# Performance work log

Hardware: AMD Instinct MI355X
Metric: run time of the kernel (lower is better)

## Reference

```python
import jax, jax.numpy as jnp
import numpy as np

IN_DIM = 256
OUT_DIM = 256
B, N, E = 8, 1024, 262144
K_RATIO = 0.5
BN_EPS = 1e-5


def _xavier(key, shape):
    fan_in, fan_out = shape[1], shape[0]
    lim = float(np.sqrt(6.0 / (fan_in + fan_out)))
    return jax.random.uniform(key, shape, jnp.float32, -lim, lim)


def setup_inputs() -> dict:
    key = jax.random.key(0)
    ks = jax.random.split(key, 10)
    x = jax.random.normal(ks[0], (B, N, IN_DIM), jnp.float32)
    edges = jax.random.randint(ks[1], (2, E), 0, B * N, jnp.int64 if jax.config.jax_enable_x64 else jnp.int32)
    return {
        "x": x,
        "edges": edges,
        "att_proj_w": _xavier(ks[2], (OUT_DIM, IN_DIM)),
        "att_proj_b": jnp.zeros((OUT_DIM,), jnp.float32),
        "att_map_w": _xavier(ks[3], (1, OUT_DIM)).reshape(OUT_DIM),
        "pwa_w": _xavier(ks[4], (OUT_DIM, IN_DIM)),
        "pwa_b": jnp.zeros((OUT_DIM,), jnp.float32),
        "pwo_w": _xavier(ks[5], (OUT_DIM, IN_DIM)),
        "pwo_b": jnp.zeros((OUT_DIM,), jnp.float32),
        "bn_gamma": jnp.ones((OUT_DIM,), jnp.float32),
        "bn_beta": jnp.zeros((OUT_DIM,), jnp.float32),
        "y_w": _xavier(ks[6], (1, OUT_DIM)).reshape(OUT_DIM),
        "y_b": jnp.zeros((), jnp.float32),
    }


def reference(x, edges, att_proj_w, att_proj_b, att_map_w, pwa_w, pwa_b,
              pwo_w, pwo_b, bn_gamma, bn_beta, y_w, y_b):
    b, n, d = x.shape
    num_nodes = b * n
    xf = x.reshape(num_nodes, d)
    src, dst = edges[0], edges[1]  # x_j = source, x_i = destination

    # --- GAT message: alpha = att_map(tanh(att_proj(x_i * x_j))) ---
    x_j = xf[src]                                # [E, d]
    x_i = xf[dst]                                # [E, d]
    h = jnp.tanh((x_i * x_j) @ att_proj_w.T + att_proj_b)  # [E, out]
    alpha = h @ att_map_w                        # [E]

    # --- segment softmax over destination nodes ---
    amax = jax.ops.segment_max(alpha, dst, num_segments=num_nodes)
    a = jnp.exp(alpha - amax[dst])
    denom = jax.ops.segment_sum(a, dst, num_segments=num_nodes)
    w = a / (denom[dst] + 1e-16)

    # --- scatter-sum aggregate of alpha * x_j ---
    agg = jax.ops.segment_sum(w[:, None] * x_j, dst, num_segments=num_nodes)  # [num_nodes, d]

    out = agg @ pwa_w.T + pwa_b + xf @ pwo_w.T + pwo_b  # [num_nodes, out]

    # --- BatchNorm1d (training-mode batch stats, biased var) + SELU ---
    mean = out.mean(axis=0)
    var = out.var(axis=0)
    out = (out - mean) * jax.lax.rsqrt(var + BN_EPS) * bn_gamma + bn_beta
    out = jax.nn.selu(out)

    out = out.reshape(b, n, -1)  # [B, N, out]

    # --- GraphPool: top-k by sigmoid score, gate by score ---
    y = jax.nn.sigmoid(out @ y_w + y_b)  # [B, N]
    k = max(int(n * K_RATIO), 1)
    vals, ids = jax.lax.top_k(y, k)      # [B, k]
    x_top = jnp.take_along_axis(out, ids[..., None], axis=1)  # [B, k, out]
    return x_top * vals[..., None]
```

## Files before the change

### kernel.cpp

```cpp
#include <hip/hip_runtime.h>
#include <math.h>

#define NODES 8192
#define NEDGE 262144
#define DIM 256

typedef float f32x16 __attribute__((ext_vector_type(16)));
typedef _Float16 f16x8 __attribute__((ext_vector_type(8)));
typedef unsigned short u16;
typedef u16 u16x8 __attribute__((ext_vector_type(8)));
typedef u16 u16x4 __attribute__((ext_vector_type(4)));
typedef u16 u16x2 __attribute__((ext_vector_type(2)));

__device__ __forceinline__ float fast_tanh(float x) {
    float t = __expf(2.f * x);
    return 1.f - 2.f * __builtin_amdgcn_rcpf(t + 1.f);
}

__device__ __forceinline__ u16 h_bits(_Float16 h) {
    u16 r; __builtin_memcpy(&r, &h, 2); return r;
}

__global__ void k_zero(int* __restrict__ deg) {
    int i = blockIdx.x * blockDim.x + threadIdx.x;
    if (i < NODES) deg[i] = 0;
}

__global__ void k_deg(const int* __restrict__ dst, int* __restrict__ deg) {
    int e = blockIdx.x * blockDim.x + threadIdx.x;
    if (e < NEDGE) atomicAdd(&deg[dst[e]], 1);
}

__global__ void k_scan(const int* __restrict__ deg, int* __restrict__ rowptr,
                       int* __restrict__ cursor) {
    __shared__ int part[256];
    int t = threadIdx.x;
    int base = t * 32;
    int local[32];
    int s = 0;
    for (int i = 0; i < 32; ++i) { local[i] = s; s += deg[base + i]; }
    part[t] = s;
    __syncthreads();
    for (int off = 1; off < 256; off <<= 1) {
        int v = (t >= off) ? part[t - off] : 0;
        __syncthreads();
        part[t] += v;
        __syncthreads();
    }
    int excl = (t == 0) ? 0 : part[t - 1];
    for (int i = 0; i < 32; ++i) {
        int v = excl + local[i];
        rowptr[base + i] = v;
        cursor[base + i] = v;
    }
    if (t == 255) rowptr[NODES] = part[255];
}

__global__ void k_fill(const int* __restrict__ src, const int* __restrict__ dst,
                       int* __restrict__ cursor, int2* __restrict__ sdg) {
    int e = blockIdx.x * blockDim.x + threadIdx.x;
    if (e < NEDGE) {
        int pos = atomicAdd(&cursor[dst[e]], 1);
        sdg[pos] = make_int2(src[e], dst[e]);
    }
}

__global__ void k_wfrag(const float* __restrict__ W, u16* __restrict__ wf) {
    int t = blockIdx.x * blockDim.x + threadIdx.x;
    if (t >= 16 * 4 * 2 * 64) return;
    int lane = t & 63;
    int mt = (t >> 6) & 1;
    int w = (t >> 7) & 3;
    int gks = t >> 9;
    int row = w * 64 + mt * 32 + (lane & 31);
    int k0 = gks * 16 + (lane >> 5) * 8;
    const float* p = W + (size_t)row * DIM + k0;
    u16x8 v1, v2;
#pragma unroll
    for (int j = 0; j < 8; ++j) {
        float f = p[j];
        _Float16 h1 = (_Float16)f;
        _Float16 h2 = (_Float16)((f - (float)h1) * 2048.f);
        v1[j] = h_bits(h1);
        v2[j] = h_bits(h2);
    }
    size_t base = ((size_t)(gks * 4 + w) * 4 + mt * 2) * 512 + lane * 8;
    *(u16x8*)(wf + base)       = v1;
    *(u16x8*)(wf + base + 512) = v2;
}

__global__ void k_wfrag2(const float* __restrict__ Wa, const float* __restrict__ Wo,
                         u16* __restrict__ wf2) {
    int t = blockIdx.x * blockDim.x + threadIdx.x;
    if (t >= 32 * 4 * 2 * 64) return;
    int lane = t & 63;
    int mt = (t >> 6) & 1;
    int w = (t >> 7) & 3;
    int gks = t >> 9;
    const float* W = (gks < 16) ? Wa : Wo;
    int row = w * 64 + mt * 32 + (lane & 31);
    int k0 = (gks & 15) * 16 + (lane >> 5) * 8;
    const float* p = W + (size_t)row * DIM + k0;
    u16x8 v1, v2;
#pragma unroll
    for (int j = 0; j < 8; ++j) {
        float f = p[j];
        _Float16 h1 = (_Float16)f;
        _Float16 h2 = (_Float16)((f - (float)h1) * 2048.f);
        v1[j] = h_bits(h1);
        v2[j] = h_bits(h2);
    }
    size_t base = ((size_t)(gks * 4 + w) * 4 + mt * 2) * 512 + lane * 8;
    *(u16x8*)(wf2 + base)       = v1;
    *(u16x8*)(wf2 + base + 512) = v2;
}

__global__ __launch_bounds__(256, 2) void k_alpha_v11(
    const float* __restrict__ x, const int2* __restrict__ sdg,
    const u16* __restrict__ wf, const float* __restrict__ bias,
    const float* __restrict__ amap, float* __restrict__ alpha_pos)
{
    __shared__ u16 p_lds[2][64][128];
    const int tid = threadIdx.x;
    const int w = tid >> 6;
    const int lane = tid & 63;
    const int l31 = lane & 31;
    const int g2 = lane >> 5;
    const int bid = blockIdx.x;
    const int wg = (bid & 7) * 512 + (bid >> 3);
    const int e0 = wg * 64;
    const int ebase = e0 + w * 16;
    const unsigned swz = ((unsigned)(l31 & 7)) << 4;

    f32x16 accM[2][2], accC[2][2];
#pragma unroll
    for (int mt = 0; mt < 2; ++mt)
#pragma unroll
        for (int nt = 0; nt < 2; ++nt) { accM[mt][nt] = (f32x16)0.f; accC[mt][nt] = (f32x16)0.f; }

    f16x8 afA[2][2], afB[2][2];

#define PREFA(DST, GKS) { \
    const u16* pb_ = wf + ((size_t)((GKS) * 4 + w) * 4) * 512 + lane * 8; \
    _Pragma("unroll") for (int mt_ = 0; mt_ < 2; ++mt_) \
    _Pragma("unroll") for (int pl_ = 0; pl_ < 2; ++pl_) \
        DST[mt_][pl_] = *(const f16x8*)(const void*)(pb_ + (mt_ * 2 + pl_) * 512); }

#define STAGE(PH) { \
    _Pragma("unroll") for (int i_ = 0; i_ < 16; ++i_) { \
        int2 sd_ = sdg[ebase + i_]; \
        float2 a_ = *(const float2*)(x + (size_t)sd_.x * DIM + (PH) * 128 + lane * 2); \
        float2 b_ = *(const float2*)(x + (size_t)sd_.y * DIM + (PH) * 128 + lane * 2); \
        float p0_ = a_.x * b_.x; \
        float p1_ = a_.y * b_.y; \
        _Float16 h10_ = (_Float16)p0_; \
        _Float16 h11_ = (_Float16)p1_; \
        _Float16 h20_ = (_Float16)((p0_ - (float)h10_) * 2048.f); \
        _Float16 h21_ = (_Float16)((p1_ - (float)h11_) * 2048.f); \
        u16x2 v1_, v2_; \
        v1_[0] = h_bits(h10_); v1_[1] = h_bits(h11_); \
        v2_[0] = h_bits(h20_); v2_[1] = h_bits(h21_); \
        const int le_ = w * 16 + i_; \
        const unsigned off_ = ((unsigned)(lane * 4)) ^ (((unsigned)(le_ & 7)) << 4); \
        *(u16x2*)((char*)&p_lds[0][le_][0] + off_) = v1_; \
        *(u16x2*)((char*)&p_lds[1][le_][0] + off_) = v2_; } }

#define KSTEP(GKS) { \
    if ((GKS) + 1 < 16) { \
        if ((GKS) & 1) { PREFA(afA, (GKS) + 1) } else { PREFA(afB, (GKS) + 1) } \
    } \
    f16x8 bfr[2][2]; \
    _Pragma("unroll") for (int nt_ = 0; nt_ < 2; ++nt_) { \
        const int en_ = nt_ * 32 + l31; \
        const unsigned off_ = ((unsigned)(((GKS) & 7) * 32 + g2 * 16)) ^ swz; \
        _Pragma("unroll") for (int pl_ = 0; pl_ < 2; ++pl_) \
            bfr[nt_][pl_] = *(const f16x8*)(const void*)((const char*)&p_lds[pl_][en_][0] + off_); \
    } \
    _Pragma("unroll") for (int mt_ = 0; mt_ < 2; ++mt_) \
    _Pragma("unroll") for (int nt_ = 0; nt_ < 2; ++nt_) { \
        f16x8 a1_ = ((GKS) & 1) ? afB[mt_][0] : afA[mt_][0]; \
        f16x8 a2_ = ((GKS) & 1) ? afB[mt_][1] : afA[mt_][1]; \
        accM[mt_][nt_] = __builtin_amdgcn_mfma_f32_32x32x16_f16(a1_, bfr[nt_][0], accM[mt_][nt_], 0, 0, 0); \
        accC[mt_][nt_] = __builtin_amdgcn_mfma_f32_32x32x16_f16(a1_, bfr[nt_][1], accC[mt_][nt_], 0, 0, 0); \
        accC[mt_][nt_] = __builtin_amdgcn_mfma_f32_32x32x16_f16(a2_, bfr[nt_][0], accC[mt_][nt_], 0, 0, 0); } }

    PREFA(afA, 0)
    STAGE(0)
    __syncthreads();
    KSTEP(0) KSTEP(1) KSTEP(2) KSTEP(3)
    KSTEP(4) KSTEP(5) KSTEP(6) KSTEP(7)
    __syncthreads();
    STAGE(1)
    __syncthreads();
    KSTEP(8)  KSTEP(9)  KSTEP(10) KSTEP(11)
    KSTEP(12) KSTEP(13) KSTEP(14) KSTEP(15)
#undef STAGE
#undef KSTEP
#undef PREFA

    float part[2] = {0.f, 0.f};
#pragma unroll
    for (int mt = 0; mt < 2; ++mt)
#pragma unroll
        for (int r = 0; r < 16; ++r) {
            int o = 64 * w + 32 * mt + (r & 3) + 8 * (r >> 2) + 4 * g2;
            float bo = bias[o], ao = amap[o];
#pragma unroll
            for (int nt = 0; nt < 2; ++nt) {
                float h = accM[mt][nt][r] + accC[mt][nt][r] * 4.8828125e-4f;
                part[nt] += ao * fast_tanh(h + bo);
            }
        }
    __syncthreads();
    float* red = (float*)(void*)p_lds;
#pragma unroll
    for (int nt = 0; nt < 2; ++nt) {
        float p = part[nt];
        p += __shfl_xor(p, 32);
        if (lane < 32) red[w * 64 + nt * 32 + lane] = p;
    }
    __syncthreads();
    if (tid < 64) alpha_pos[e0 + tid] = red[tid] + red[64 + tid] + red[128 + tid] + red[192 + tid];
}

__global__ void k_aggregate(
    const float* __restrict__ x, const float* __restrict__ alpha_pos,
    const int* __restrict__ rowptr, const int2* __restrict__ sdg,
    float* __restrict__ agg)
{
    int gw = (blockIdx.x * blockDim.x + threadIdx.x) >> 6;
    int lane = threadIdx.x & 63;
    if (gw >= NODES) return;
    int start = rowptr[gw], end = rowptr[gw + 1];
    int deg = end - start;
    float m = -INFINITY;
    for (int i = lane; i < deg; i += 64) m = fmaxf(m, alpha_pos[start + i]);
#pragma unroll
    for (int off = 32; off > 0; off >>= 1) m = fmaxf(m, __shfl_xor(m, off));
    float ssum = 0.f;
    for (int i = lane; i < deg; i += 64) ssum += expf(alpha_pos[start + i] - m);
#pragma unroll
    for (int off = 32; off > 0; off >>= 1) ssum += __shfl_xor(ssum, off);
    float a0 = 0.f, a1 = 0.f, a2 = 0.f, a3 = 0.f;
    int i = 0;
    for (; i + 4 <= deg; i += 4) {
        float w0 = expf(alpha_pos[start + i]     - m);
        float w1 = expf(alpha_pos[start + i + 1] - m);
        float w2 = expf(alpha_pos[start + i + 2] - m);
        float w3 = expf(alpha_pos[start + i + 3] - m);
        int r0 = sdg[start + i].x;
        int r1 = sdg[start + i + 1].x;
        int r2 = sdg[start + i + 2].x;
        int r3 = sdg[start + i + 3].x;
        float4 v0 = *(const float4*)(x + (size_t)r0 * DIM + lane * 4);
        float4 v1 = *(const float4*)(x + (size_t)r1 * DIM + lane * 4);
        float4 v2 = *(const float4*)(x + (size_t)r2 * DIM + lane * 4);
        float4 v3 = *(const float4*)(x + (size_t)r3 * DIM + lane * 4);
        a0 += w0 * v0.x + w1 * v1.x + w2 * v2.x + w3 * v3.x;
        a1 += w0 * v0.y + w1 * v1.y + w2 * v2.y + w3 * v3.y;
        a2 += w0 * v0.z + w1 * v1.z + w2 * v2.z + w3 * v3.z;
        a3 += w0 * v0.w + w1 * v1.w + w2 * v2.w + w3 * v3.w;
    }
    for (; i < deg; ++i) {
        float wgt = expf(alpha_pos[start + i] - m);
        int r = sdg[start + i].x;
        const float4 v = *(const float4*)(x + (size_t)r * DIM + lane * 4);
        a0 += wgt * v.x; a1 += wgt * v.y; a2 += wgt * v.z; a3 += wgt * v.w;
    }
    float inv = 1.f / (ssum + 1e-16f);
    float4 r; r.x = a0 * inv; r.y = a1 * inv; r.z = a2 * inv; r.w = a3 * inv;
    *(float4*)(agg + (size_t)gw * DIM + lane * 4) = r;
}

__global__ __launch_bounds__(256, 2) void k_out_mfma(
    const float* __restrict__ agg, const float* __restrict__ x,
    const u16* __restrict__ wf2, const float* __restrict__ ba,
    const float* __restrict__ bo, float* __restrict__ outb)
{
    __shared__ u16 p_lds[2][64][256];
    const int tid = threadIdx.x;
    const int w = tid >> 6;
    const int lane = tid & 63;
    const int l31 = lane & 31;
    const int g2 = lane >> 5;
    const int n0 = blockIdx.x * 64;
    const unsigned swz = ((unsigned)(l31 & 7)) << 4;

    f32x16 accM[2][2], accC[2][2];
#pragma unroll
    for (int mt = 0; mt < 2; ++mt)
#pragma unroll
        for (int nt = 0; nt < 2; ++nt) { accM[mt][nt] = (f32x16)0.f; accC[mt][nt] = (f32x16)0.f; }

    f16x8 afA[2][2], afB[2][2];

#define PREFA2(DST, GKS) { \
    const u16* pb_ = wf2 + ((size_t)((GKS) * 4 + w) * 4) * 512 + lane * 8; \
    _Pragma("unroll") for (int mt_ = 0; mt_ < 2; ++mt_) \
    _Pragma("unroll") for (int pl_ = 0; pl_ < 2; ++pl_) \
        DST[mt_][pl_] = *(const f16x8*)(const void*)(pb_ + (mt_ * 2 + pl_) * 512); }

#define OSTAGE(SRC) { \
    _Pragma("unroll") for (int i_ = 0; i_ < 16; ++i_) { \
        const int ln_ = w * 16 + i_; \
        float4 v_ = *(const float4*)((SRC) + (size_t)(n0 + ln_) * DIM + lane * 4); \
        float pv_[4] = {v_.x, v_.y, v_.z, v_.w}; \
        u16x4 v1_, v2_; \
        _Pragma("unroll") for (int j_ = 0; j_ < 4; ++j_) { \
            float f_ = pv_[j_]; \
            _Float16 h1_ = (_Float16)f_; \
            _Float16 h2_ = (_Float16)((f_ - (float)h1_) * 2048.f); \
            v1_[j_] = h_bits(h1_); v2_[j_] = h_bits(h2_); } \
        const unsigned off_ = ((unsigned)(lane * 8)) ^ (((unsigned)(ln_ & 7)) << 4); \
        *(u16x4*)((char*)&p_lds[0][ln_][0] + off_) = v1_; \
        *(u16x4*)((char*)&p_lds[1][ln_][0] + off_) = v2_; } }

#define OKSTEP(GKS) { \
    if ((GKS) + 1 < 32) { \
        if ((GKS) & 1) { PREFA2(afA, (GKS) + 1) } else { PREFA2(afB, (GKS) + 1) } \
    } \
    f16x8 bfr[2][2]; \
    _Pragma("unroll") for (int nt_ = 0; nt_ < 2; ++nt_) { \
        const int en_ = nt_ * 32 + l31; \
        const unsigned off_ = ((unsigned)(((GKS) & 15) * 32 + g2 * 16)) ^ swz; \
        _Pragma("unroll") for (int pl_ = 0; pl_ < 2; ++pl_) \
            bfr[nt_][pl_] = *(const f16x8*)(const void*)((const char*)&p_lds[pl_][en_][0] + off_); \
    } \
    _Pragma("unroll") for (int mt_ = 0; mt_ < 2; ++mt_) \
    _Pragma("unroll") for (int nt_ = 0; nt_ < 2; ++nt_) { \
        f16x8 a1_ = ((GKS) & 1) ? afB[mt_][0] : afA[mt_][0]; \
        f16x8 a2_ = ((GKS) & 1) ? afB[mt_][1] : afA[mt_][1]; \
        accM[mt_][nt_] = __builtin_amdgcn_mfma_f32_32x32x16_f16(a1_, bfr[nt_][0], accM[mt_][nt_], 0, 0, 0); \
        accC[mt_][nt_] = __builtin_amdgcn_mfma_f32_32x32x16_f16(a1_, bfr[nt_][1], accC[mt_][nt_], 0, 0, 0); \
        accC[mt_][nt_] = __builtin_amdgcn_mfma_f32_32x32x16_f16(a2_, bfr[nt_][0], accC[mt_][nt_], 0, 0, 0); } }

    PREFA2(afA, 0)
    OSTAGE(agg)
    __syncthreads();
    OKSTEP(0)  OKSTEP(1)  OKSTEP(2)  OKSTEP(3)
    OKSTEP(4)  OKSTEP(5)  OKSTEP(6)  OKSTEP(7)
    OKSTEP(8)  OKSTEP(9)  OKSTEP(10) OKSTEP(11)
    OKSTEP(12) OKSTEP(13) OKSTEP(14) OKSTEP(15)
    __syncthreads();
    OSTAGE(x)
    __syncthreads();
    OKSTEP(16) OKSTEP(17) OKSTEP(18) OKSTEP(19)
    OKSTEP(20) OKSTEP(21) OKSTEP(22) OKSTEP(23)
    OKSTEP(24) OKSTEP(25) OKSTEP(26) OKSTEP(27)
    OKSTEP(28) OKSTEP(29) OKSTEP(30) OKSTEP(31)
#undef OSTAGE
#undef OKSTEP
#undef PREFA2

    __syncthreads();
    float* Cs = (float*)(void*)p_lds;
#pragma unroll
    for (int mt = 0; mt < 2; ++mt)
#pragma unroll
        for (int r = 0; r < 16; ++r) {
            int o = 64 * w + 32 * mt + (r & 3) + 8 * (r >> 2) + 4 * g2;
            float bs = ba[o] + bo[o];
#pragma unroll
            for (int nt = 0; nt < 2; ++nt) {
                int col = nt * 32 + l31;
                float hv = accM[mt][nt][r] + accC[mt][nt][r] * 4.8828125e-4f + bs;
                unsigned ob = ((unsigned)(col * 1024 + o * 4)) ^ (((unsigned)(col & 31)) << 4);
                *(float*)((char*)Cs + ob) = hv;
            }
        }
    __syncthreads();
#pragma unroll
    for (int i = 0; i < 16; ++i) {
        int ln = w * 16 + i;
        unsigned rb = ((unsigned)(ln * 1024 + lane * 16)) ^ (((unsigned)(ln & 31)) << 4);
        float4 val = *(const float4*)((const char*)Cs + rb);
        *(float4*)(outb + (size_t)(n0 + ln) * DIM + lane * 4) = val;
    }
}

__global__ void k_colstat(const float* __restrict__ outb, double* __restrict__ psum,
                          double* __restrict__ psq) {
    int g = blockIdx.x, t = threadIdx.x;
    double s = 0.0, q = 0.0;
    const float* p = outb + (size_t)g * 256 * DIM + t;
    for (int r = 0; r < 256; ++r) { double v = (double)p[(size_t)r * DIM]; s += v; q += v * v; }
    psum[g * DIM + t] = s;
    psq[g * DIM + t] = q;
}

__global__ void k_bnparam(const double* __restrict__ psum, const double* __restrict__ psq,
                          const float* __restrict__ gamma, const float* __restrict__ beta,
                          float* __restrict__ scale, float* __restrict__ shift) {
    int t = threadIdx.x;
    double s = 0.0, q = 0.0;
    for (int g = 0; g < 32; ++g) { s += psum[g * DIM + t]; q += psq[g * DIM + t]; }
    double mean = s / (double)NODES;
    double var = q / (double)NODES - mean * mean;
    float sc = (float)((double)gamma[t] / sqrt(var + 1e-5));
    scale[t] = sc;
    shift[t] = (float)((double)beta[t] - mean * (double)sc);
}

__global__ void k_bnselu(float* __restrict__ outb, const float* __restrict__ scale,
                         const float* __restrict__ shift, const float* __restrict__ yw,
                         const float* __restrict__ yb, float* __restrict__ y) {
    int gw = (blockIdx.x * blockDim.x + threadIdx.x) >> 6;
    int lane = threadIdx.x & 63;
    if (gw >= NODES) return;
    float4 v  = *(const float4*)(outb + (size_t)gw * DIM + lane * 4);
    float4 sc = *(const float4*)(scale + lane * 4);
    float4 sh = *(const float4*)(shift + lane * 4);
    const float SL = 1.0507009873554805f, SA = 1.6732632423543772f;
    float4 o;
    o.x = v.x * sc.x + sh.x;
    o.y = v.y * sc.y + sh.y;
    o.z = v.z * sc.z + sh.z;
    o.w = v.w * sc.w + sh.w;
    o.x = (o.x > 0.f) ? SL * o.x : SL * SA * expm1f(o.x);
    o.y = (o.y > 0.f) ? SL * o.y : SL * SA * expm1f(o.y);
    o.z = (o.z > 0.f) ? SL * o.z : SL * SA * expm1f(o.z);
    o.w = (o.w > 0.f) ? SL * o.w : SL * SA * expm1f(o.w);
    *(float4*)(outb + (size_t)gw * DIM + lane * 4) = o;
    float4 w = *(const float4*)(yw + lane * 4);
    float z = o.x * w.x + o.y * w.y + o.z * w.z + o.w * w.w;
#pragma unroll
    for (int off = 32; off > 0; off >>= 1) z += __shfl_xor(z, off);
    if (lane == 0) y[gw] = 1.f / (1.f + expf(-(z + yb[0])));
}

__global__ void k_topk(const float* __restrict__ y, float* __restrict__ svals,
                       int* __restrict__ sidx) {
    __shared__ float v[1024];
    __shared__ int  id[1024];
    int b = blockIdx.x, t = threadIdx.x;
    v[t] = y[b * 1024 + t];           id[t] = t;
    v[t + 512] = y[b * 1024 + t + 512]; id[t + 512] = t + 512;
    __syncthreads();
    for (int k = 2; k <= 1024; k <<= 1) {
        for (int j = k >> 1; j > 0; j >>= 1) {
            for (int i = t; i < 1024; i += 512) {
                int l = i ^ j;
                if (l > i) {
                    float vi = v[i], vl = v[l];
                    int ii = id[i], il = id[l];
                    bool precede = (vi > vl) || (vi == vl && ii < il);
                    bool dirDesc = ((i & k) == 0);
                    bool sw = dirDesc ? !precede : precede;
                    if (sw) { v[i] = vl; v[l] = vi; id[i] = il; id[l] = ii; }
                }
            }
            __syncthreads();
        }
    }
    if (t < 512) { svals[b * 512 + t] = v[t]; sidx[b * 512 + t] = id[t]; }
}

__global__ void k_gather(const float* __restrict__ outb, const float* __restrict__ svals,
                         const int* __restrict__ sidx, float* __restrict__ dout) {
    int gw = (blockIdx.x * blockDim.x + threadIdx.x) >> 6;
    int lane = threadIdx.x & 63;
    int b = gw >> 9, r = gw & 511;
    float val = svals[b * 512 + r];
    int idn = sidx[b * 512 + r];
    float4 vv = *(const float4*)(outb + (size_t)(b * 1024 + idn) * DIM + lane * 4);
    vv.x *= val; vv.y *= val; vv.z *= val; vv.w *= val;
    *(float4*)(dout + (size_t)(b * 512 + r) * DIM + lane * 4) = vv;
}

extern "C" void kernel_launch(void* const* d_in, const int* in_sizes, int n_in,
                              void* d_out, int out_size, void* d_ws, size_t ws_size,
                              hipStream_t stream) {
    const float* x     = (const float*)d_in[0];
    const int* edges   = (const int*)d_in[1];
    const float* att_w = (const float*)d_in[2];
    const float* att_b = (const float*)d_in[3];
    const float* amap  = (const float*)d_in[4];
    const float* pwa_w = (const float*)d_in[5];
    const float* pwa_b = (const float*)d_in[6];
    const float* pwo_w = (const float*)d_in[7];
    const float* pwo_b = (const float*)d_in[8];
    const float* gamma = (const float*)d_in[9];
    const float* beta  = (const float*)d_in[10];
    const float* yw    = (const float*)d_in[11];
    const float* yb    = (const float*)d_in[12];
    float* out = (float*)d_out;
    const int* src = edges;
    const int* dst = edges + NEDGE;

    char* ws = (char*)d_ws;
    size_t off = 0;
    auto alloc = [&](size_t b) { void* p = ws + off; off = (off + b + 255) & ~(size_t)255; return p; };
    float* alpha  = (float*)alloc((size_t)NEDGE * 4);
    int2*  sdg    = (int2*)alloc((size_t)NEDGE * 8);
    float* agg    = (float*)alloc((size_t)NODES * DIM * 4);
    float* outb   = (float*)alloc((size_t)NODES * DIM * 4);
    int*   deg    = (int*)alloc(NODES * 4);
    int*   rowptr = (int*)alloc((NODES + 1) * 4);
    int*   cursor = (int*)alloc(NODES * 4);
    double* psum  = (double*)alloc(32 * DIM * 8);
    double* psq   = (double*)alloc(32 * DIM * 8);
    float* scale  = (float*)alloc(DIM * 4);
    float* shift  = (float*)alloc(DIM * 4);
    float* yv     = (float*)alloc(NODES * 4);
    float* svals  = (float*)alloc(8 * 512 * 4);
    int*   sidx   = (int*)alloc(8 * 512 * 4);
    u16*   wf     = (u16*)alloc((size_t)16 * 4 * 4 * 512 * 2);
    u16*   wf2    = (u16*)alloc((size_t)32 * 4 * 4 * 512 * 2);

    k_wfrag<<<32, 256, 0, stream>>>(att_w, wf);
    k_wfrag2<<<64, 256, 0, stream>>>(pwa_w, pwo_w, wf2);
    k_zero<<<NODES / 256, 256, 0, stream>>>(deg);
    k_deg<<<NEDGE / 256, 256, 0, stream>>>(dst, deg);
    k_scan<<<1, 256, 0, stream>>>(deg, rowptr, cursor);
    k_fill<<<NEDGE / 256, 256, 0, stream>>>(src, dst, cursor, sdg);
    k_alpha_v11<<<NEDGE / 64, 256, 0, stream>>>(x, sdg, wf, att_b, amap, alpha);
    k_aggregate<<<NODES / 4, 256, 0, stream>>>(x, alpha, rowptr, sdg, agg);
    k_out_mfma<<<NODES / 64, 256, 0, stream>>>(agg, x, wf2, pwa_b, pwo_b, outb);
    k_colstat<<<32, 256, 0, stream>>>(outb, psum, psq);
    k_bnparam<<<1, 256, 0, stream>>>(psum, psq, gamma, beta, scale, shift);
    k_bnselu<<<NODES / 4, 256, 0, stream>>>(outb, scale, shift, yw, yb, yv);
    k_topk<<<8, 512, 0, stream>>>(yv, svals, sidx);
    k_gather<<<(8 * 512) / 4, 256, 0, stream>>>(outb, svals, sidx, out);
}
```

Measured before the change: 274.8 us.

## Stage full K in LDS once and triple-buffer weight fragment prefetch

The alpha kernel now stages the whole 256-wide edge product (hi/lo fp16 split) into a doubled LDS buffer in one pass using float4 gathers, removing the second staging phase and two barriers. Weight fragment prefetch moves from double to triple buffering with a distance of two k-steps. The zero kernel is replaced with hipMemsetAsync. LDS use doubles to 64KB per block, which may limit the intended 2 blocks per CU, and the extra fragment registers raise register pressure.

```diff
diff --git a/kernel.cpp b/kernel.cpp
--- a/kernel.cpp
+++ b/kernel.cpp
@@ -10,7 +10,6 @@
 typedef unsigned short u16;
 typedef u16 u16x8 __attribute__((ext_vector_type(8)));
 typedef u16 u16x4 __attribute__((ext_vector_type(4)));
-typedef u16 u16x2 __attribute__((ext_vector_type(2)));
 
 __device__ __forceinline__ float fast_tanh(float x) {
     float t = __expf(2.f * x);
@@ -19,11 +18,6 @@
 
 __device__ __forceinline__ u16 h_bits(_Float16 h) {
     u16 r; __builtin_memcpy(&r, &h, 2); return r;
-}
-
-__global__ void k_zero(int* __restrict__ deg) {
-    int i = blockIdx.x * blockDim.x + threadIdx.x;
-    if (i < NODES) deg[i] = 0;
 }
 
 __global__ void k_deg(const int* __restrict__ dst, int* __restrict__ deg) {
@@ -115,12 +109,12 @@
     *(u16x8*)(wf2 + base + 512) = v2;
 }
 
-__global__ __launch_bounds__(256, 2) void k_alpha_v11(
+__global__ __launch_bounds__(256, 2) void k_alpha_v12(
     const float* __restrict__ x, const int2* __restrict__ sdg,
     const u16* __restrict__ wf, const float* __restrict__ bias,
     const float* __restrict__ amap, float* __restrict__ alpha_pos)
 {
-    __shared__ u16 p_lds[2][64][128];
+    __shared__ u16 p_lds[2][64][256];
     const int tid = threadIdx.x;
     const int w = tid >> 6;
     const int lane = tid & 63;
@@ -138,7 +132,7 @@
 #pragma unroll
         for (int nt = 0; nt < 2; ++nt) { accM[mt][nt] = (f32x16)0.f; accC[mt][nt] = (f32x16)0.f; }
 
-    f16x8 afA[2][2], afB[2][2];
+    f16x8 afA[2][2], afB[2][2], afC[2][2];
 
 #define PREFA(DST, GKS) { \
     const u16* pb_ = wf + ((size_t)((GKS) * 4 + w) * 4) * 512 + lane * 8; \
@@ -146,56 +140,53 @@
     _Pragma("unroll") for (int pl_ = 0; pl_ < 2; ++pl_) \
         DST[mt_][pl_] = *(const f16x8*)(const void*)(pb_ + (mt_ * 2 + pl_) * 512); }
 
-#define STAGE(PH) { \
-    _Pragma("unroll") for (int i_ = 0; i_ < 16; ++i_) { \
-        int2 sd_ = sdg[ebase + i_]; \
-        float2 a_ = *(const float2*)(x + (size_t)sd_.x * DIM + (PH) * 128 + lane * 2); \
-        float2 b_ = *(const float2*)(x + (size_t)sd_.y * DIM + (PH) * 128 + lane * 2); \
-        float p0_ = a_.x * b_.x; \
-        float p1_ = a_.y * b_.y; \
-        _Float16 h10_ = (_Float16)p0_; \
-        _Float16 h11_ = (_Float16)p1_; \
-        _Float16 h20_ = (_Float16)((p0_ - (float)h10_) * 2048.f); \
-        _Float16 h21_ = (_Float16)((p1_ - (float)h11_) * 2048.f); \
-        u16x2 v1_, v2_; \
-        v1_[0] = h_bits(h10_); v1_[1] = h_bits(h11_); \
-        v2_[0] = h_bits(h20_); v2_[1] = h_bits(h21_); \
-        const int le_ = w * 16 + i_; \
-        const unsigned off_ = ((unsigned)(lane * 4)) ^ (((unsigned)(le_ & 7)) << 4); \
-        *(u16x2*)((char*)&p_lds[0][le_][0] + off_) = v1_; \
-        *(u16x2*)((char*)&p_lds[1][le_][0] + off_) = v2_; } }
-
-#define KSTEP(GKS) { \
-    if ((GKS) + 1 < 16) { \
-        if ((GKS) & 1) { PREFA(afA, (GKS) + 1) } else { PREFA(afB, (GKS) + 1) } \
-    } \
+#define KS(GKS, USE, PF) { \
+    if ((GKS) + 2 < 16) { PREFA(PF, (GKS) + 2) } \
     f16x8 bfr[2][2]; \
     _Pragma("unroll") for (int nt_ = 0; nt_ < 2; ++nt_) { \
         const int en_ = nt_ * 32 + l31; \
-        const unsigned off_ = ((unsigned)(((GKS) & 7) * 32 + g2 * 16)) ^ swz; \
+        const unsigned off_ = ((unsigned)((GKS) * 32 + g2 * 16)) ^ swz; \
         _Pragma("unroll") for (int pl_ = 0; pl_ < 2; ++pl_) \
             bfr[nt_][pl_] = *(const f16x8*)(const void*)((const char*)&p_lds[pl_][en_][0] + off_); \
     } \
     _Pragma("unroll") for (int mt_ = 0; mt_ < 2; ++mt_) \
     _Pragma("unroll") for (int nt_ = 0; nt_ < 2; ++nt_) { \
-        f16x8 a1_ = ((GKS) & 1) ? afB[mt_][0] : afA[mt_][0]; \
-        f16x8 a2_ = ((GKS) & 1) ? afB[mt_][1] : afA[mt_][1]; \
-        accM[mt_][nt_] = __builtin_amdgcn_mfma_f32_32x32x16_f16(a1_, bfr[nt_][0], accM[mt_][nt_], 0, 0, 0); \
-        accC[mt_][nt_] = __builtin_amdgcn_mfma_f32_32x32x16_f16(a1_, bfr[nt_][1], accC[mt_][nt_], 0, 0, 0); \
-        accC[mt_][nt_] = __builtin_amdgcn_mfma_f32_32x32x16_f16(a2_, bfr[nt_][0], accC[mt_][nt_], 0, 0, 0); } }
+        accM[mt_][nt_] = __builtin_amdgcn_mfma_f32_32x32x16_f16(USE[mt_][0], bfr[nt_][0], accM[mt_][nt_], 0, 0, 0); \
+        accC[mt_][nt_] = __builtin_amdgcn_mfma_f32_32x32x16_f16(USE[mt_][0], bfr[nt_][1], accC[mt_][nt_], 0, 0, 0); \
+        accC[mt_][nt_] = __builtin_amdgcn_mfma_f32_32x32x16_f16(USE[mt_][1], bfr[nt_][0], accC[mt_][nt_], 0, 0, 0); } }
 
     PREFA(afA, 0)
-    STAGE(0)
-    __syncthreads();
-    KSTEP(0) KSTEP(1) KSTEP(2) KSTEP(3)
-    KSTEP(4) KSTEP(5) KSTEP(6) KSTEP(7)
-    __syncthreads();
-    STAGE(1)
-    __syncthreads();
-    KSTEP(8)  KSTEP(9)  KSTEP(10) KSTEP(11)
-    KSTEP(12) KSTEP(13) KSTEP(14) KSTEP(15)
-#undef STAGE
-#undef KSTEP
+    PREFA(afB, 1)
+
+#pragma unroll
+    for (int i = 0; i < 16; ++i) {
+        int2 sd = sdg[ebase + i];
+        float4 a = *(const float4*)(x + (size_t)sd.x * DIM + lane * 4);
+        float4 b = *(const float4*)(x + (size_t)sd.y * DIM + lane * 4);
+        float pv[4] = {a.x * b.x, a.y * b.y, a.z * b.z, a.w * b.w};
+        u16x4 v1, v2;
+#pragma unroll
+        for (int j = 0; j < 4; ++j) {
+            float f = pv[j];
+            _Float16 h1 = (_Float16)f;
+            _Float16 h2 = (_Float16)((f - (float)h1) * 2048.f);
+            v1[j] = h_bits(h1);
+            v2[j] = h_bits(h2);
+        }
+        const int le = w * 16 + i;
+        const unsigned off = ((unsigned)(lane * 8)) ^ (((unsigned)(le & 7)) << 4);
+        *(u16x4*)((char*)&p_lds[0][le][0] + off) = v1;
+        *(u16x4*)((char*)&p_lds[1][le][0] + off) = v2;
+    }
+    __syncthreads();
+
+    KS(0,  afA, afC) KS(1,  afB, afA) KS(2,  afC, afB)
+    KS(3,  afA, afC) KS(4,  afB, afA) KS(5,  afC, afB)
+    KS(6,  afA, afC) KS(7,  afB, afA) KS(8,  afC, afB)
+    KS(9,  afA, afC) KS(10, afB, afA) KS(11, afC, afB)
+    KS(12, afA, afC) KS(13, afB, afA) KS(14, afC, afB)
+    KS(15, afA, afC)
+#undef KS
 #undef PREFA
 
     float part[2] = {0.f, 0.f};
@@ -507,13 +498,13 @@
     u16*   wf     = (u16*)alloc((size_t)16 * 4 * 4 * 512 * 2);
     u16*   wf2    = (u16*)alloc((size_t)32 * 4 * 4 * 512 * 2);
 
+    hipMemsetAsync(deg, 0, NODES * 4, stream);
     k_wfrag<<<32, 256, 0, stream>>>(att_w, wf);
     k_wfrag2<<<64, 256, 0, stream>>>(pwa_w, pwo_w, wf2);
-    k_zero<<<NODES / 256, 256, 0, stream>>>(deg);
     k_deg<<<NEDGE / 256, 256, 0, stream>>>(dst, deg);
     k_scan<<<1, 256, 0, stream>>>(deg, rowptr, cursor);
     k_fill<<<NEDGE / 256, 256, 0, stream>>>(src, dst, cursor, sdg);
-    k_alpha_v11<<<NEDGE / 64, 256, 0, stream>>>(x, sdg, wf, att_b, amap, alpha);
+    k_alpha_v12<<<NEDGE / 64, 256, 0, stream>>>(x, sdg, wf, att_b, amap, alpha);
     k_aggregate<<<NODES / 4, 256, 0, stream>>>(x, alpha, rowptr, sdg, agg);
     k_out_mfma<<<NODES / 64, 256, 0, stream>>>(agg, x, wf2, pwa_b, pwo_b, outb);
     k_colstat<<<32, 256, 0, stream>>>(outb, psum, psq);
```

Result: faster. 266.5 us (-3.0%).
